# Kernel optimization log

Hardware: AMD Instinct MI355X
Metric: run time of the kernel (lower is better)

## Reference

```python
import jax, jax.numpy as jnp
import numpy as np

N = 50000
F = 96
E = 800000
H = 2
DEPTH = 3
LEAKY_ALPHA = 0.2  # tf.nn.leaky_relu default


def setup_inputs() -> dict:
    key = jax.random.key(0)
    k1, k2, k3, k4, k5, k6 = jax.random.split(key, 6)
    node_f = jax.random.normal(k1, (N, F), dtype=jnp.float32)
    rows = jax.random.randint(k2, (E,), 0, N, dtype=jnp.int64)
    cols = jax.random.randint(k3, (E,), 0, N, dtype=jnp.int64)
    adj_idx = jnp.stack([rows, cols], axis=-1)[None]  # [1, E, 2]
    diag = jnp.arange(N, dtype=jnp.int64)
    adj_self_idx = jnp.stack([diag, diag], axis=-1)  # [N, 2] self loops
    adj_self_val = jax.random.uniform(k4, (N,), dtype=jnp.float32)
    attn_self_k = jax.random.normal(k5, (H, F), dtype=jnp.float32) * 0.05
    attn_neigh_k = jax.random.normal(k6, (H, F), dtype=jnp.float32) * 0.05
    return {"node_f": node_f, "adj_idx": adj_idx, "adj_self_idx": adj_self_idx,
            "adj_self_val": adj_self_val, "attn_self_k": attn_self_k,
            "attn_neigh_k": attn_neigh_k}


def _segment_softmax(scores, seg, n):
    # softmax over the nonzero entries of each row (tf.sparse_softmax semantics)
    m = jax.ops.segment_max(scores, seg, num_segments=n)
    ex = jnp.exp(scores - m[seg])
    denom = jax.ops.segment_sum(ex, seg, num_segments=n)
    return ex / denom[seg]


def reference(node_f, adj_idx, adj_self_idx, adj_self_val, attn_self_k, attn_neigh_k):
    rows = adj_idx[0, :, 0]
    cols = adj_idx[0, :, 1]
    s_rows = adj_self_idx[:, 0]
    s_cols = adj_self_idx[:, 1]
    # features = adj_self @ node_f (sparse matmul)
    features = jax.ops.segment_sum(adj_self_val[:, None] * node_f[s_cols],
                                   s_rows, num_segments=N)
    features = jax.nn.relu(features)
    outputs = [features]
    for _ in range(DEPTH):
        def head_fn(a_s, a_n, feats=features):
            e_self = feats @ a_s    # [N]
            e_neigh = feats @ a_n   # [N]
            scores = jax.nn.leaky_relu(e_self[rows] + e_neigh[cols], LEAKY_ALPHA)
            att = _segment_softmax(scores, rows, N)  # [E]
            return jax.ops.segment_sum(att[:, None] * feats[cols], rows,
                                       num_segments=N)  # [N, F]
        heads = jax.vmap(head_fn)(attn_self_k, attn_neigh_k)  # [H, N, F]
        features = jax.nn.relu(jnp.mean(heads, axis=0))
        outputs.append(features)
    return jnp.concatenate(outputs, axis=-1)  # [N, F*(DEPTH+1)]
```

## Files before the change

kernel.cpp:

```cpp
#include <hip/hip_runtime.h>
#include <math.h>

#define NN 50000
#define FF 96
#define EE 800000
#define OF 384
#define GB 3125
#define FBU 48
#define CAP 64
#define NB 196
#define BCAP 4608
#define CHUNK 4082
#define SHARD 12500

__device__ __forceinline__ float grp_sum(float v) {
    for (int m = 8; m >= 1; m >>= 1) v += __shfl_xor(v, m, 64);
    return v;
}
__device__ __forceinline__ float grp_max(float v) {
    for (int m = 8; m >= 1; m >>= 1) v = fmaxf(v, __shfl_xor(v, m, 64));
    return v;
}
__device__ __forceinline__ float lrelu(float x) { return x > 0.f ? x : 0.2f * x; }
__device__ __forceinline__ void online_upd(float s, float& m, float& d) {
    float nm = fmaxf(m, s);
    d = d * __expf(m - nm) + __expf(s - nm);
    m = nm;
}
__device__ __forceinline__ float bf_lo(unsigned u) { return __uint_as_float(u << 16); }
__device__ __forceinline__ float bf_hi(unsigned u) { return __uint_as_float(u & 0xffff0000u); }
__device__ __forceinline__ unsigned pack_bf(float a, float b) {
    unsigned ua = __float_as_uint(a), ub = __float_as_uint(b);
    ua = ua + 0x7fffu + ((ua >> 16) & 1u);
    ub = ub + 0x7fffu + ((ub >> 16) & 1u);
    return (ua >> 16) | (ub & 0xffff0000u);
}

__device__ __forceinline__ float grp_dot8(const float* a,
                                          const float* __restrict__ kf, int lg) {
    float s = 0.f;
    if (lg < 12) {
        float4 w0 = ((const float4*)kf)[2 * lg];
        float4 w1 = ((const float4*)kf)[2 * lg + 1];
        s = a[0] * w0.x + a[1] * w0.y + a[2] * w0.z + a[3] * w0.w +
            a[4] * w1.x + a[5] * w1.y + a[6] * w1.z + a[7] * w1.w;
    }
    return grp_sum(s);
}

template<int BF>
__global__ __launch_bounds__(256) void l0_phase1(const float* __restrict__ node_f,
                                                 const int* __restrict__ sidx,
                                                 const float* __restrict__ sval,
                                                 float* __restrict__ out,
                                                 unsigned* __restrict__ fb,
                                                 const float* __restrict__ ks,
                                                 const float* __restrict__ kn,
                                                 float2* __restrict__ ass,
                                                 float2* __restrict__ ann,
                                                 const int2* __restrict__ idx2,
                                                 int* __restrict__ bfill,
                                                 unsigned* __restrict__ buckets) {
    __shared__ int cnt[NB], basearr[NB], ofs[NB];
    int tid = threadIdx.x;
    if (blockIdx.x >= GB) {
        int p = blockIdx.x - GB;
        int start = p * CHUNK, end = min(start + CHUNK, EE);
        if (tid < NB) { cnt[tid] = 0; ofs[tid] = 0; }
        __syncthreads();
        for (int e = start + tid; e < end; e += 256)
            atomicAdd(&cnt[idx2[e].x >> 8], 1);
        __syncthreads();
        if (tid < NB)
            basearr[tid] = cnt[tid] ? atomicAdd(&bfill[tid], cnt[tid]) : 0;
        __syncthreads();
        for (int e = start + tid; e < end; e += 256) {
            int2 q = idx2[e];
            int b = q.x >> 8;
            int slot = basearr[b] + atomicAdd(&ofs[b], 1);
            if (slot < BCAP)
                buckets[(size_t)b * BCAP + slot] =
                    ((unsigned)(q.x & 255) << 16) | (unsigned)q.y;
        }
        return;
    }
    int g = tid >> 4, lg = tid & 15;
    int n = blockIdx.x * 16 + g;
    if (n >= NN) return;
    int sr = sidx[2 * n];
    int sc = sidx[2 * n + 1];
    float v = sval[n];
    float a[8] = {0.f, 0.f, 0.f, 0.f, 0.f, 0.f, 0.f, 0.f};
    if (lg < 12) {
        const float4* xr4 = (const float4*)(node_f + (size_t)sc * FF);
        float4 x0 = xr4[2 * lg], x1 = xr4[2 * lg + 1];
        a[0] = fmaxf(v * x0.x, 0.f); a[1] = fmaxf(v * x0.y, 0.f);
        a[2] = fmaxf(v * x0.z, 0.f); a[3] = fmaxf(v * x0.w, 0.f);
        a[4] = fmaxf(v * x1.x, 0.f); a[5] = fmaxf(v * x1.y, 0.f);
        a[6] = fmaxf(v * x1.z, 0.f); a[7] = fmaxf(v * x1.w, 0.f);
        float4* op4 = (float4*)(out + (size_t)sr * OF);
        op4[2 * lg]     = make_float4(a[0], a[1], a[2], a[3]);
        op4[2 * lg + 1] = make_float4(a[4], a[5], a[6], a[7]);
        if (BF) {
            uint4 p;
            p.x = pack_bf(a[0], a[1]); p.y = pack_bf(a[2], a[3]);
            p.z = pack_bf(a[4], a[5]); p.w = pack_bf(a[6], a[7]);
            ((uint4*)(fb + (size_t)sr * FBU))[lg] = p;
        }
    }
    float p0 = grp_dot8(a, ks, lg);
    float p1 = grp_dot8(a, ks + FF, lg);
    float p2 = grp_dot8(a, kn, lg);
    float p3 = grp_dot8(a, kn + FF, lg);
    if (lg == 0) {
        ass[sr] = make_float2(p0, p1);
        ann[sr] = make_float2(p2, p3);
    }
}

__global__ __launch_bounds__(256) void bucket2csr(const int* __restrict__ bfill,
                                                  const unsigned* __restrict__ buckets,
                                                  int* __restrict__ fill,
                                                  unsigned short* __restrict__ csr) {
    __shared__ unsigned short lcsr[256 * CAP];
    __shared__ int lcnt[256 * 4], loff[256 * 4];
    int tid = threadIdx.x, b = blockIdx.x;
#pragma unroll
    for (int c = 0; c < 4; ++c) lcnt[tid * 4 + c] = 0;
    __syncthreads();
    int cnt = min(bfill[b], BCAP);
    const unsigned* bp = buckets + (size_t)b * BCAP;
    for (int i = tid; i < cnt; i += 256) {
        unsigned u = bp[i];
        atomicAdd(&lcnt[(u >> 16) * 4 + (int)((u & 0xffffu) / SHARD)], 1);
    }
    __syncthreads();
    {
        int c0 = lcnt[tid * 4], c1 = lcnt[tid * 4 + 1];
        int c2 = lcnt[tid * 4 + 2], c3 = lcnt[tid * 4 + 3];
        loff[tid * 4] = 0;
        loff[tid * 4 + 1] = c0;
        loff[tid * 4 + 2] = c0 + c1;
        loff[tid * 4 + 3] = c0 + c1 + c2;
        int r = b * 256 + tid;
        if (r < NN) fill[r] = min(c0 + c1 + c2 + c3, CAP);
        lcnt[tid * 4] = 0; lcnt[tid * 4 + 1] = 0;
        lcnt[tid * 4 + 2] = 0; lcnt[tid * 4 + 3] = 0;
    }
    __syncthreads();
    for (int i = tid; i < cnt; i += 256) {
        unsigned u = bp[i];
        int lr = u >> 16, col = u & 0xffffu, cls = col / SHARD;
        int pos = loff[lr * 4 + cls] + atomicAdd(&lcnt[lr * 4 + cls], 1);
        if (pos < CAP) lcsr[lr * CAP + pos] = (unsigned short)col;
    }
    __syncthreads();
    const uint4* src = (const uint4*)lcsr;
    uint4* dst = (uint4*)(csr + (size_t)b * 256 * CAP);
    for (int i = tid; i < 256 * CAP / 8; i += 256) dst[i] = src[i];
}

template<int BF>
__device__ __forceinline__ void agg_chunk(float cj, int colj, int nj, int gbase,
                                          const float* __restrict__ feats,
                                          const unsigned* __restrict__ fb, int lg,
                                          float* a) {
#pragma unroll 8
    for (int k = 0; k < nj; ++k) {
        float cc = __shfl(cj, gbase + k, 64);
        int col  = __shfl(colj, gbase + k, 64);
        if (lg < 12) {
            if (BF) {
                uint4 q = ((const uint4*)(fb + (size_t)col * FBU))[lg];
                a[0] += cc * bf_lo(q.x); a[1] += cc * bf_hi(q.x);
                a[2] += cc * bf_lo(q.y); a[3] += cc * bf_hi(q.y);
                a[4] += cc * bf_lo(q.z); a[5] += cc * bf_hi(q.z);
                a[6] += cc * bf_lo(q.w); a[7] += cc * bf_hi(q.w);
            } else {
                const float4* vp = (const float4*)(feats + (size_t)col * OF);
                float4 v0 = vp[2 * lg], v1 = vp[2 * lg + 1];
                a[0] += cc * v0.x; a[1] += cc * v0.y;
                a[2] += cc * v0.z; a[3] += cc * v0.w;
                a[4] += cc * v1.x; a[5] += cc * v1.y;
                a[6] += cc * v1.z; a[7] += cc * v1.w;
            }
        }
    }
}

template<int BF>
__global__ __launch_bounds__(256) void gat_layer(float* __restrict__ out, int l,
                                                 const int* __restrict__ fill,
                                                 const unsigned short* __restrict__ csr,
                                                 const float2* __restrict__ ass,
                                                 const float2* __restrict__ ann,
                                                 const unsigned* __restrict__ fb_in,
                                                 unsigned* __restrict__ fb_out,
                                                 const float* __restrict__ ks,
                                                 const float* __restrict__ kn,
                                                 float2* __restrict__ ass_out,
                                                 float2* __restrict__ ann_out,
                                                 int write_dots) {
    int tid = threadIdx.x;
    int g = tid >> 4, lg = tid & 15;
    int gbase = (g & 3) * 16;
    int r = blockIdx.x * 16 + g;
    if (r >= NN) return;
    int deg = fill[r];
    const unsigned short* crow = csr + (size_t)r * CAP;
    const float* feats = out + l * FF;
    float2 as_r = ass[r];

    float m0 = -1e30f, m1 = -1e30f, d0 = 0.f, d1 = 0.f;
    int   c0col = 0, c1col = 0;
    float c0s0 = -1e30f, c0s1 = -1e30f, c1s0 = -1e30f, c1s1 = -1e30f;
    if (lg < deg) {
        int c = crow[lg];
        float2 an = ann[c];
        c0col = c;
        c0s0 = lrelu(as_r.x + an.x);
        c0s1 = lrelu(as_r.y + an.y);
        online_upd(c0s0, m0, d0);
        online_upd(c0s1, m1, d1);
    }
    if (deg > 16) {
        int j = 16 + lg;
        if (j < deg) {
            int c = crow[j];
            float2 an = ann[c];
            c1col = c;
            c1s0 = lrelu(as_r.x + an.x);
            c1s1 = lrelu(as_r.y + an.y);
            online_upd(c1s0, m0, d0);
            online_upd(c1s1, m1, d1);
        }
        for (int j0 = 32; j0 < deg; j0 += 16) {
            int jj = j0 + lg;
            if (jj < deg) {
                int c = crow[jj];
                float2 an = ann[c];
                online_upd(lrelu(as_r.x + an.x), m0, d0);
                online_upd(lrelu(as_r.y + an.y), m1, d1);
            }
        }
    }
    float M0 = grp_max(m0), M1 = grp_max(m1);
    d0 = grp_sum(d0 * __expf(m0 - M0));
    d1 = grp_sum(d1 * __expf(m1 - M1));
    float inv0 = d0 > 0.f ? 0.5f / d0 : 0.f;
    float inv1 = d1 > 0.f ? 0.5f / d1 : 0.f;

    float a[8] = {0.f, 0.f, 0.f, 0.f, 0.f, 0.f, 0.f, 0.f};
    {
        float cj = __expf(c0s0 - M0) * inv0 + __expf(c0s1 - M1) * inv1;
        agg_chunk<BF>(cj, c0col, min(deg, 16), gbase, feats, fb_in, lg, a);
    }
    if (deg > 16) {
        float cj = __expf(c1s0 - M0) * inv0 + __expf(c1s1 - M1) * inv1;
        agg_chunk<BF>(cj, c1col, min(deg - 16, 16), gbase, feats, fb_in, lg, a);
        for (int j0 = 32; j0 < deg; j0 += 16) {
            float cjr = 0.f; int colr = 0;
            int jj = j0 + lg;
            if (jj < deg) {
                int c = crow[jj];
                float2 an = ann[c];
                cjr = __expf(lrelu(as_r.x + an.x) - M0) * inv0 +
                      __expf(lrelu(as_r.y + an.y) - M1) * inv1;
                colr = c;
            }
            agg_chunk<BF>(cjr, colr, min(deg - j0, 16), gbase, feats, fb_in, lg, a);
        }
    }

#pragma unroll
    for (int i = 0; i < 8; ++i) a[i] = fmaxf(a[i], 0.f);
    if (lg < 12) {
        float4* op4 = (float4*)(out + (size_t)r * OF + (l + 1) * FF);
        op4[2 * lg]     = make_float4(a[0], a[1], a[2], a[3]);
        op4[2 * lg + 1] = make_float4(a[4], a[5], a[6], a[7]);
        if (BF && fb_out) {
            uint4 p;
            p.x = pack_bf(a[0], a[1]); p.y = pack_bf(a[2], a[3]);
            p.z = pack_bf(a[4], a[5]); p.w = pack_bf(a[6], a[7]);
            ((uint4*)(fb_out + (size_t)r * FBU))[lg] = p;
        }
    }

    if (write_dots) {
        float p0 = grp_dot8(a, ks, lg);
        float p1 = grp_dot8(a, ks + FF, lg);
        float p2 = grp_dot8(a, kn, lg);
        float p3 = grp_dot8(a, kn + FF, lg);
        if (lg == 0) {
            ass_out[r] = make_float2(p0, p1);
            ann_out[r] = make_float2(p2, p3);
        }
    }
}

extern "C" void kernel_launch(void* const* d_in, const int* in_sizes, int n_in,
                              void* d_out, int out_size, void* d_ws, size_t ws_size,
                              hipStream_t stream) {
    const float* node_f  = (const float*)d_in[0];
    const int*   adj_idx = (const int*)d_in[1];
    const int*   sidx    = (const int*)d_in[2];
    const float* sval    = (const float*)d_in[3];
    const float* k_self  = (const float*)d_in[4];
    const float* k_neigh = (const float*)d_in[5];
    float* out = (float*)d_out;

    char* w = (char*)d_ws;
    auto alloc = [&](size_t bytes) {
        char* p = w;
        w += (bytes + 255) & ~(size_t)255;
        return p;
    };
    int*            fill    = (int*)alloc((size_t)NN * 4);
    unsigned short* csr     = (unsigned short*)alloc((size_t)NB * 256 * CAP * 2);
    int*            bfill   = (int*)alloc((size_t)NB * 4);
    unsigned*       buckets = (unsigned*)alloc((size_t)NB * BCAP * 4);
    float2*         ass_a   = (float2*)alloc((size_t)NN * 8);
    float2*         ann_a   = (float2*)alloc((size_t)NN * 8);
    float2*         ass_b   = (float2*)alloc((size_t)NN * 8);
    float2*         ann_b   = (float2*)alloc((size_t)NN * 8);
    unsigned*       fb_a    = (unsigned*)alloc((size_t)NN * FBU * 4);
    unsigned*       fb_b    = (unsigned*)alloc((size_t)NN * FBU * 4);
    bool bf = (size_t)(w - (char*)d_ws) <= ws_size;

    hipMemsetAsync(bfill, 0, (size_t)NB * 4, stream);

    if (bf) {
        l0_phase1<1><<<GB + NB, 256, 0, stream>>>(node_f, sidx, sval, out, fb_a,
                                                  k_self, k_neigh, ass_a, ann_a,
                                                  (const int2*)adj_idx, bfill, buckets);
        bucket2csr<<<NB, 256, 0, stream>>>(bfill, buckets, fill, csr);
        gat_layer<1><<<GB, 256, 0, stream>>>(out, 0, fill, csr, ass_a, ann_a,
                                             fb_a, fb_b, k_self, k_neigh,
                                             ass_b, ann_b, 1);
        gat_layer<1><<<GB, 256, 0, stream>>>(out, 1, fill, csr, ass_b, ann_b,
                                             fb_b, fb_a, k_self, k_neigh,
                                             ass_a, ann_a, 1);
        gat_layer<1><<<GB, 256, 0, stream>>>(out, 2, fill, csr, ass_a, ann_a,
                                             fb_a, nullptr, k_self, k_neigh,
                                             ass_b, ann_b, 0);
    } else {
        l0_phase1<0><<<GB + NB, 256, 0, stream>>>(node_f, sidx, sval, out, nullptr,
                                                  k_self, k_neigh, ass_a, ann_a,
                                                  (const int2*)adj_idx, bfill, buckets);
        bucket2csr<<<NB, 256, 0, stream>>>(bfill, buckets, fill, csr);
        gat_layer<0><<<GB, 256, 0, stream>>>(out, 0, fill, csr, ass_a, ann_a,
                                             nullptr, nullptr, k_self, k_neigh,
                                             ass_b, ann_b, 1);
        gat_layer<0><<<GB, 256, 0, stream>>>(out, 1, fill, csr, ass_b, ann_b,
                                             nullptr, nullptr, k_self, k_neigh,
                                             ass_a, ann_a, 1);
        gat_layer<0><<<GB, 256, 0, stream>>>(out, 2, fill, csr, ass_a, ann_a,
                                             nullptr, nullptr, k_self, k_neigh,
                                             ass_b, ann_b, 0);
    }
}
```

Measured before the change: 235.5 us.

## Use finer 64-row edge buckets and schedule binning blocks first

```diff
diff --git a/kernel.cpp b/kernel.cpp
--- a/kernel.cpp
+++ b/kernel.cpp
@@ -8,9 +8,12 @@
 #define GB 3125
 #define FBU 48
 #define CAP 64
-#define NB 196
-#define BCAP 4608
-#define CHUNK 4082
+#define BSH 6
+#define BROWS 64
+#define NB 782
+#define BCAP 1536
+#define P1 800
+#define CHUNK 1000
 #define SHARD 12500
 
 __device__ __forceinline__ float grp_sum(float v) {
@@ -63,29 +66,29 @@
                                                  unsigned* __restrict__ buckets) {
     __shared__ int cnt[NB], basearr[NB], ofs[NB];
     int tid = threadIdx.x;
-    if (blockIdx.x >= GB) {
-        int p = blockIdx.x - GB;
+    if (blockIdx.x < P1) {
+        int p = blockIdx.x;
         int start = p * CHUNK, end = min(start + CHUNK, EE);
-        if (tid < NB) { cnt[tid] = 0; ofs[tid] = 0; }
+        for (int b = tid; b < NB; b += 256) { cnt[b] = 0; ofs[b] = 0; }
         __syncthreads();
         for (int e = start + tid; e < end; e += 256)
-            atomicAdd(&cnt[idx2[e].x >> 8], 1);
+            atomicAdd(&cnt[idx2[e].x >> BSH], 1);
         __syncthreads();
-        if (tid < NB)
-            basearr[tid] = cnt[tid] ? atomicAdd(&bfill[tid], cnt[tid]) : 0;
+        for (int b = tid; b < NB; b += 256)
+            basearr[b] = cnt[b] ? atomicAdd(&bfill[b], cnt[b]) : 0;
         __syncthreads();
         for (int e = start + tid; e < end; e += 256) {
             int2 q = idx2[e];
-            int b = q.x >> 8;
+            int b = q.x >> BSH;
             int slot = basearr[b] + atomicAdd(&ofs[b], 1);
             if (slot < BCAP)
                 buckets[(size_t)b * BCAP + slot] =
-                    ((unsigned)(q.x & 255) << 16) | (unsigned)q.y;
+                    ((unsigned)(q.x & (BROWS - 1)) << 16) | (unsigned)q.y;
         }
         return;
     }
     int g = tid >> 4, lg = tid & 15;
-    int n = blockIdx.x * 16 + g;
+    int n = (blockIdx.x - P1) * 16 + g;
     if (n >= NN) return;
     int sr = sidx[2 * n];
     int sc = sidx[2 * n + 1];
@@ -122,11 +125,10 @@
                                                   const unsigned* __restrict__ buckets,
                                                   int* __restrict__ fill,
                                                   unsigned short* __restrict__ csr) {
-    __shared__ unsigned short lcsr[256 * CAP];
-    __shared__ int lcnt[256 * 4], loff[256 * 4];
+    __shared__ unsigned short lcsr[BROWS * CAP];
+    __shared__ int lcnt[BROWS * 4], loff[BROWS * 4];
     int tid = threadIdx.x, b = blockIdx.x;
-#pragma unroll
-    for (int c = 0; c < 4; ++c) lcnt[tid * 4 + c] = 0;
+    lcnt[tid] = 0;
     __syncthreads();
     int cnt = min(bfill[b], BCAP);
     const unsigned* bp = buckets + (size_t)b * BCAP;
@@ -135,14 +137,14 @@
         atomicAdd(&lcnt[(u >> 16) * 4 + (int)((u & 0xffffu) / SHARD)], 1);
     }
     __syncthreads();
-    {
+    if (tid < BROWS) {
         int c0 = lcnt[tid * 4], c1 = lcnt[tid * 4 + 1];
         int c2 = lcnt[tid * 4 + 2], c3 = lcnt[tid * 4 + 3];
         loff[tid * 4] = 0;
         loff[tid * 4 + 1] = c0;
         loff[tid * 4 + 2] = c0 + c1;
         loff[tid * 4 + 3] = c0 + c1 + c2;
-        int r = b * 256 + tid;
+        int r = b * BROWS + tid;
         if (r < NN) fill[r] = min(c0 + c1 + c2 + c3, CAP);
         lcnt[tid * 4] = 0; lcnt[tid * 4 + 1] = 0;
         lcnt[tid * 4 + 2] = 0; lcnt[tid * 4 + 3] = 0;
@@ -156,8 +158,8 @@
     }
     __syncthreads();
     const uint4* src = (const uint4*)lcsr;
-    uint4* dst = (uint4*)(csr + (size_t)b * 256 * CAP);
-    for (int i = tid; i < 256 * CAP / 8; i += 256) dst[i] = src[i];
+    uint4* dst = (uint4*)(csr + (size_t)b * BROWS * CAP);
+    for (int i = tid; i < BROWS * CAP / 8; i += 256) dst[i] = src[i];
 }
 
 template<int BF>
@@ -316,7 +318,7 @@
         return p;
     };
     int*            fill    = (int*)alloc((size_t)NN * 4);
-    unsigned short* csr     = (unsigned short*)alloc((size_t)NB * 256 * CAP * 2);
+    unsigned short* csr     = (unsigned short*)alloc((size_t)NB * BROWS * CAP * 2);
     int*            bfill   = (int*)alloc((size_t)NB * 4);
     unsigned*       buckets = (unsigned*)alloc((size_t)NB * BCAP * 4);
     float2*         ass_a   = (float2*)alloc((size_t)NN * 8);
@@ -330,7 +332,7 @@
     hipMemsetAsync(bfill, 0, (size_t)NB * 4, stream);
 
     if (bf) {
-        l0_phase1<1><<<GB + NB, 256, 0, stream>>>(node_f, sidx, sval, out, fb_a,
+        l0_phase1<1><<<P1 + GB, 256, 0, stream>>>(node_f, sidx, sval, out, fb_a,
                                                   k_self, k_neigh, ass_a, ann_a,
                                                   (const int2*)adj_idx, bfill, buckets);
         bucket2csr<<<NB, 256, 0, stream>>>(bfill, buckets, fill, csr);
@@ -344,7 +346,7 @@
                                              fb_a, nullptr, k_self, k_neigh,
                                              ass_b, ann_b, 0);
     } else {
-        l0_phase1<0><<<GB + NB, 256, 0, stream>>>(node_f, sidx, sval, out, nullptr,
+        l0_phase1<0><<<P1 + GB, 256, 0, stream>>>(node_f, sidx, sval, out, nullptr,
                                                   k_self, k_neigh, ass_a, ann_a,
                                                   (const int2*)adj_idx, bfill, buckets);
         bucket2csr<<<NB, 256, 0, stream>>>(bfill, buckets, fill, csr);
```

Measured after the change: 246.2 us. 1.05x slower.
